# Kernel tuning notes

Measured on AMD Instinct MI355X. Metric: run time of the kernel, lower is better.

Reference implementation:

```python
import jax, jax.numpy as jnp
import numpy as np

B, C, H, W, D = 2, 256, 16, 16, 16
CQK = C // 8  # 32


def setup_inputs() -> dict:
    key = jax.random.key(0)
    ks = jax.random.split(key, 6)
    x = jax.random.normal(ks[0], (B, C, H, W, D), dtype=jnp.float32)
    wq = jax.random.normal(ks[1], (CQK, C), dtype=jnp.float32) * (1.0 / np.sqrt(C))
    wk = jax.random.normal(ks[2], (CQK, C), dtype=jnp.float32) * (1.0 / np.sqrt(C))
    wv = jax.random.normal(ks[3], (C, C), dtype=jnp.float32) * (1.0 / np.sqrt(C))
    bq = jnp.zeros((CQK,), dtype=jnp.float32)
    bk = jnp.zeros((CQK,), dtype=jnp.float32)
    bv = jnp.zeros((C,), dtype=jnp.float32)
    gamma_pam = jax.random.normal(ks[4], (1,), dtype=jnp.float32)
    gamma_cam = jax.random.normal(ks[5], (1,), dtype=jnp.float32)
    return {"x": x, "wq": wq, "bq": bq, "wk": wk, "bk": bk,
            "wv": wv, "bv": bv, "gamma_pam": gamma_pam, "gamma_cam": gamma_cam}


def _da_block(x, wq, bq, wk, bk, wv, bv, gamma_pam, gamma_cam):
    b, c, h, w, d = x.shape
    n = h * w * d
    xf = x.reshape(b, c, n)  # (B, C, N)

    # ---- PAM (position attention) ----
    # 1x1x1 Conv3d == per-voxel channel matmul
    q = jnp.einsum('oc,bcn->bon', wq, xf) + bq[None, :, None]  # (B, CQK, N)
    k = jnp.einsum('oc,bcn->bon', wk, xf) + bk[None, :, None]  # (B, CQK, N)
    v = jnp.einsum('oc,bcn->bon', wv, xf) + bv[None, :, None]  # (B, C, N)
    energy = jnp.einsum('bci,bcj->bij', q, k)                  # (B, N, N)
    attn = jax.nn.softmax(energy, axis=-1)
    # out[b,c,i] = sum_j v[b,c,j] * attn[b,i,j]
    pam_out = jnp.einsum('bcj,bij->bci', v, attn)              # (B, C, N)
    x1 = gamma_pam[0] * pam_out.reshape(b, c, h, w, d) + x

    # ---- CAM (channel attention, max-inverted energy) ----
    energy_c = jnp.einsum('bin,bjn->bij', xf, xf)              # (B, C, C)
    energy_new = jnp.max(energy_c, axis=-1, keepdims=True) - energy_c
    attn_c = jax.nn.softmax(energy_new, axis=-1)
    cam_out = jnp.einsum('bij,bjn->bin', attn_c, xf)           # (B, C, N)
    x2 = gamma_cam[0] * cam_out.reshape(b, c, h, w, d) + x

    return x1 + x2


def reference(x, wq, bq, wk, bk, wv, bv, gamma_pam, gamma_cam):
    return _da_block(x, wq, bq, wk, bk, wv, bv, gamma_pam, gamma_cam)
```

## Files before the change

### kernel.cpp

```cpp
#include <hip/hip_runtime.h>
#include <hip/hip_bf16.h>


#define B_ 2
#define C_ 256
#define N_ 4096
#define QK_ 32

#define TJ_ 128
#define PPB_ 136

typedef __hip_bfloat16 bf16;
typedef __attribute__((ext_vector_type(8))) short bf16x8f;
typedef __attribute__((ext_vector_type(4))) float f32x4;

union bf8pack { bf16 h[8]; int4 v; bf16x8f f; };
union bf4pack { bf16 h[4]; uint2 u; };

__global__ __launch_bounds__(256) void k_wcv(
    const float* __restrict__ wq, const float* __restrict__ wk, const float* __restrict__ wv,
    bf16* __restrict__ wqkh, bf16* __restrict__ wqkl,
    bf16* __restrict__ wvh, bf16* __restrict__ wvl) {
  int idx = blockIdx.x * 256 + threadIdx.x;
  if (idx < 64 * C_) {
    int r = idx >> 8, c = idx & 255;
    float v = (r < 32) ? wq[r * C_ + c] : wk[(r - 32) * C_ + c];
    bf16 h = __float2bfloat16(v);
    wqkh[idx] = h; wqkl[idx] = __float2bfloat16(v - __bfloat162float(h));
  } else {
    int j = idx - 64 * C_;
    float v = wv[j];
    bf16 h = __float2bfloat16(v);
    wvh[j] = h; wvl[j] = __float2bfloat16(v - __bfloat162float(h));
  }
}

__global__ __launch_bounds__(256) void k_xt(
    const float* __restrict__ x, bf16* __restrict__ xthi, bf16* __restrict__ xtlo,
    bf16* __restrict__ xchi, bf16* __restrict__ xclo) {
  int b = blockIdx.z;
  int c0 = blockIdx.y * 64;
  int n0 = blockIdx.x * 64;
  __shared__ float t[64 * 65];
  int tid = threadIdx.x;
  int col = tid & 63, rowq = tid >> 6;
#pragma unroll
  for (int k = 0; k < 16; k++) {
    int r = k * 4 + rowq;
    size_t src = ((size_t)b * C_ + c0 + r) * N_ + n0 + col;
    float v = x[src];
    t[r * 65 + col] = v;
    bf16 h = __float2bfloat16(v);
    xchi[src] = h;
    xclo[src] = __float2bfloat16(v - __bfloat162float(h));
  }
  __syncthreads();
#pragma unroll
  for (int k = 0; k < 16; k++) {
    int nrow = k * 4 + rowq;
    float v = t[col * 65 + nrow];
    bf16 h = __float2bfloat16(v);
    size_t o = ((size_t)b * N_ + n0 + nrow) * C_ + c0 + col;
    xthi[o] = h;
    xtlo[o] = __float2bfloat16(v - __bfloat162float(h));
  }
}

__global__ __launch_bounds__(256) void k_qkp(
    const bf16* __restrict__ xthi, const bf16* __restrict__ xtlo,
    const bf16* __restrict__ wqkh, const bf16* __restrict__ wqkl,
    const float* __restrict__ bq, const float* __restrict__ bk,
    bf16* __restrict__ qhi, bf16* __restrict__ qlo,
    bf16* __restrict__ khi, bf16* __restrict__ klo) {
  int b = blockIdx.y;
  int tid = threadIdx.x;
  int lane = tid & 63, wave = tid >> 6;
  int n16 = lane & 15, quad = lane >> 4;
  int nb = blockIdx.x * 32;

  f32x4 acc[2];
#pragma unroll
  for (int nt = 0; nt < 2; nt++) acc[nt] = (f32x4)(0.f);

#pragma unroll
  for (int kk = 0; kk < 8; kk++) {
    bf16x8f Ah, Al, Bh[2], Bl[2];
    {
      size_t off = (size_t)(wave * 16 + n16) * C_ + kk * 32 + quad * 8;
      Ah = *(const bf16x8f*)(const void*)(wqkh + off);
      Al = *(const bf16x8f*)(const void*)(wqkl + off);
    }
#pragma unroll
    for (int nt = 0; nt < 2; nt++) {
      size_t off = ((size_t)b * N_ + nb + nt * 16 + n16) * C_ + kk * 32 + quad * 8;
      Bh[nt] = *(const bf16x8f*)(const void*)(xthi + off);
      Bl[nt] = *(const bf16x8f*)(const void*)(xtlo + off);
    }
#pragma unroll
    for (int nt = 0; nt < 2; nt++) {
      acc[nt] = __builtin_amdgcn_mfma_f32_16x16x32_bf16(Ah, Bh[nt], acc[nt], 0, 0, 0);
      acc[nt] = __builtin_amdgcn_mfma_f32_16x16x32_bf16(Al, Bh[nt], acc[nt], 0, 0, 0);
      acc[nt] = __builtin_amdgcn_mfma_f32_16x16x32_bf16(Ah, Bl[nt], acc[nt], 0, 0, 0);
    }
  }
#pragma unroll
  for (int nt = 0; nt < 2; nt++) {
    int n = nb + nt * 16 + n16;
    int o0 = (wave & 1) * 16 + quad * 4;
    bf4pack ph, pl;
#pragma unroll
    for (int r = 0; r < 4; r++) {
      float v = acc[nt][r] + (wave < 2 ? bq[o0 + r] : bk[o0 + r]);
      bf16 h = __float2bfloat16(v);
      ph.h[r] = h; pl.h[r] = __float2bfloat16(v - __bfloat162float(h));
    }
    size_t base = ((size_t)b * N_ + n) * QK_ + o0;
    if (wave < 2) { *(uint2*)(qhi + base) = ph.u; *(uint2*)(qlo + base) = pl.u; }
    else          { *(uint2*)(khi + base) = ph.u; *(uint2*)(klo + base) = pl.u; }
  }
}

__global__ __launch_bounds__(256) void k_vbf2(
    const bf16* __restrict__ xthi, const bf16* __restrict__ xtlo,
    const bf16* __restrict__ wvh, const bf16* __restrict__ wvl,
    const float* __restrict__ bv, bf16* __restrict__ vbf) {
  int b = blockIdx.y;
  int n0 = blockIdx.x * 32;
  int tid = threadIdx.x;
  int lane = tid & 63, wave = tid >> 6;
  int n16 = lane & 15, quad = lane >> 4;
  int c0 = wave * 64;

  f32x4 acc[4][2];
#pragma unroll
  for (int ct = 0; ct < 4; ct++)
#pragma unroll
    for (int nt = 0; nt < 2; nt++) acc[ct][nt] = (f32x4)(0.f);

#pragma unroll
  for (int kk = 0; kk < 8; kk++) {
    bf16x8f Ah[4], Al[4], Bh[2], Bl[2];
#pragma unroll
    for (int ct = 0; ct < 4; ct++) {
      size_t off = (size_t)(c0 + ct * 16 + n16) * C_ + kk * 32 + quad * 8;
      Ah[ct] = *(const bf16x8f*)(const void*)(wvh + off);
      Al[ct] = *(const bf16x8f*)(const void*)(wvl + off);
    }
#pragma unroll
    for (int nt = 0; nt < 2; nt++) {
      size_t off = ((size_t)b * N_ + n0 + nt * 16 + n16) * C_ + kk * 32 + quad * 8;
      Bh[nt] = *(const bf16x8f*)(const void*)(xthi + off);
      Bl[nt] = *(const bf16x8f*)(const void*)(xtlo + off);
    }
#pragma unroll
    for (int ct = 0; ct < 4; ct++)
#pragma unroll
      for (int nt = 0; nt < 2; nt++) {
        acc[ct][nt] = __builtin_amdgcn_mfma_f32_16x16x32_bf16(Ah[ct], Bh[nt], acc[ct][nt], 0, 0, 0);
        acc[ct][nt] = __builtin_amdgcn_mfma_f32_16x16x32_bf16(Al[ct], Bh[nt], acc[ct][nt], 0, 0, 0);
        acc[ct][nt] = __builtin_amdgcn_mfma_f32_16x16x32_bf16(Ah[ct], Bl[nt], acc[ct][nt], 0, 0, 0);
      }
  }
#pragma unroll
  for (int ct = 0; ct < 4; ct++)
#pragma unroll
    for (int nt = 0; nt < 2; nt++) {
      int n = n0 + nt * 16 + n16;
      int cb = c0 + ct * 16 + quad * 4;
#pragma unroll
      for (int r = 0; r < 4; r++) {
        float v = acc[ct][nt][r] + bv[cb + r];
        vbf[((size_t)b * C_ + cb + r) * N_ + n] = __float2bfloat16(v);
      }
    }
}

__global__ __launch_bounds__(512) void k_pbm(
    const bf16* __restrict__ qhi, const bf16* __restrict__ qlo,
    const bf16* __restrict__ khi, const bf16* __restrict__ klo,
    const bf16* __restrict__ vbf,
    float* __restrict__ pamT) {
  int b = blockIdx.z;
  int h0 = blockIdx.y * 128;
  int i0 = blockIdx.x * 64;
  int tid = threadIdx.x;
  int lane = tid & 63, wave = tid >> 6;
  int n16 = lane & 15, quad = lane >> 4;

  __shared__ __align__(16) bf16 p_s[2][64 * PPB_];

  bf16x8f ahf[4], alf[4];
#pragma unroll
  for (int ih = 0; ih < 4; ih++) {
    size_t qoff = ((size_t)b * N_ + i0 + ih * 16 + n16) * QK_ + quad * 8;
    ahf[ih] = *(const bf16x8f*)(const void*)(qhi + qoff);
    alf[ih] = *(const bf16x8f*)(const void*)(qlo + qoff);
  }

  f32x4 acc[4];
  float l16[16];
#pragma unroll
  for (int ih = 0; ih < 4; ih++) acc[ih] = (f32x4)(0.f);
#pragma unroll
  for (int k = 0; k < 16; k++) l16[k] = 0.f;

  const bf16* khb = khi + ((size_t)b * N_ + wave * 16 + n16) * QK_ + quad * 8;
  const bf16* klb = klo + ((size_t)b * N_ + wave * 16 + n16) * QK_ + quad * 8;
  const bf16* vb0 = vbf + ((size_t)b * C_ + h0 + wave * 16 + n16) * N_ + quad * 8;

  const int NJT = N_ / TJ_;

  bf16x8f khf = *(const bf16x8f*)(const void*)khb;
  bf16x8f klf = *(const bf16x8f*)(const void*)klb;
  {
    bf16* pbuf = p_s[0];
#pragma unroll
    for (int ih = 0; ih < 4; ih++) {
      f32x4 t = (f32x4)(0.f);
      t = __builtin_amdgcn_mfma_f32_16x16x32_bf16(ahf[ih], khf, t, 0, 0, 0);
      t = __builtin_amdgcn_mfma_f32_16x16x32_bf16(alf[ih], khf, t, 0, 0, 0);
      t = __builtin_amdgcn_mfma_f32_16x16x32_bf16(ahf[ih], klf, t, 0, 0, 0);
#pragma unroll
      for (int r = 0; r < 4; r++) {
        int i = ih * 16 + quad * 4 + r;
        float p = __expf(t[r]);
        l16[ih * 4 + r] += p;
        pbuf[i * PPB_ + wave * 16 + n16] = __float2bfloat16(p);
      }
    }
  }
  khf = *(const bf16x8f*)(const void*)(khb + (size_t)TJ_ * QK_);
  klf = *(const bf16x8f*)(const void*)(klb + (size_t)TJ_ * QK_);
  bf16x8f vcur[4];
#pragma unroll
  for (int jhh = 0; jhh < 4; jhh++)
    vcur[jhh] = *(const bf16x8f*)(const void*)(vb0 + jhh * 32);
  __syncthreads();

  for (int jt = 0; jt < NJT; jt++) {
    f32x4 z[4];
    if (jt + 1 < NJT) {
#pragma unroll
      for (int ih = 0; ih < 4; ih++) {
        f32x4 t = (f32x4)(0.f);
        t = __builtin_amdgcn_mfma_f32_16x16x32_bf16(ahf[ih], khf, t, 0, 0, 0);
        t = __builtin_amdgcn_mfma_f32_16x16x32_bf16(alf[ih], khf, t, 0, 0, 0);
        t = __builtin_amdgcn_mfma_f32_16x16x32_bf16(ahf[ih], klf, t, 0, 0, 0);
        z[ih] = t;
      }
    }
    {
      const bf16* pbuf = p_s[jt & 1];
#pragma unroll
      for (int jhh = 0; jhh < 4; jhh++) {
        bf16x8f pa[4];
#pragma unroll
        for (int ih = 0; ih < 4; ih++)
          pa[ih] = *(const bf16x8f*)(const void*)(pbuf + (ih * 16 + n16) * PPB_ + jhh * 32 + quad * 8);
#pragma unroll
        for (int ih = 0; ih < 4; ih++)
          acc[ih] = __builtin_amdgcn_mfma_f32_16x16x32_bf16(pa[ih], vcur[jhh], acc[ih], 0, 0, 0);
      }
    }
    if (jt + 1 < NJT) {
      bf16* pbuf = p_s[(jt + 1) & 1];
#pragma unroll
      for (int ih = 0; ih < 4; ih++)
#pragma unroll
        for (int r = 0; r < 4; r++) {
          int i = ih * 16 + quad * 4 + r;
          float p = __expf(z[ih][r]);
          l16[ih * 4 + r] += p;
          pbuf[i * PPB_ + wave * 16 + n16] = __float2bfloat16(p);
        }
    }
    bf16x8f khn, kln, vnxt[4];
    if (jt + 2 < NJT) {
      size_t koff = (size_t)(jt + 2) * TJ_ * QK_;
      khn = *(const bf16x8f*)(const void*)(khb + koff);
      kln = *(const bf16x8f*)(const void*)(klb + koff);
    }
    if (jt + 1 < NJT) {
      int jb = (jt + 1) * TJ_;
#pragma unroll
      for (int jhh = 0; jhh < 4; jhh++)
        vnxt[jhh] = *(const bf16x8f*)(const void*)(vb0 + jb + jhh * 32);
    }
    __syncthreads();
    khf = khn; klf = kln;
#pragma unroll
    for (int jhh = 0; jhh < 4; jhh++) vcur[jhh] = vnxt[jhh];
  }

#pragma unroll
  for (int d = 1; d < 16; d <<= 1)
#pragma unroll
    for (int k = 0; k < 16; k++)
      l16[k] += __shfl_xor(l16[k], d, 64);
  float* red = (float*)p_s;
  float* linv = red + 8 * 64;
  if (n16 == 0) {
#pragma unroll
    for (int ih = 0; ih < 4; ih++)
#pragma unroll
      for (int r = 0; r < 4; r++)
        red[wave * 64 + ih * 16 + quad * 4 + r] = l16[ih * 4 + r];
  }
  __syncthreads();
  if (tid < 64) {
    float L = 0.f;
#pragma unroll
    for (int w = 0; w < 8; w++) L += red[w * 64 + tid];
    linv[tid] = 1.0f / L;
  }
  __syncthreads();
  int c = h0 + wave * 16 + n16;
#pragma unroll
  for (int ih = 0; ih < 4; ih++)
#pragma unroll
    for (int r = 0; r < 4; r++) {
      int i = ih * 16 + quad * 4 + r;
      pamT[((size_t)b * N_ + i0 + i) * C_ + c] = acc[ih][r] * linv[i];
    }
}

__global__ __launch_bounds__(256) void k_ce2(
    const bf16* __restrict__ xchi, const bf16* __restrict__ xclo,
    float* __restrict__ eCp) {
  int b = blockIdx.z;
  int kc = blockIdx.y;
  int it = blockIdx.x & 7, jh = blockIdx.x >> 3;
  int i0 = it * 32;
  int tid = threadIdx.x;
  int lane = tid & 63, wave = tid >> 6;
  int n16 = lane & 15, quad = lane >> 4;
  int j0 = jh * 128 + wave * 32;

  f32x4 acc[2][2];
#pragma unroll
  for (int it2 = 0; it2 < 2; it2++)
#pragma unroll
    for (int jt = 0; jt < 2; jt++) acc[it2][jt] = (f32x4)(0.f);

  size_t kb = (size_t)kc * 512;
#pragma unroll 2
  for (int kk = 0; kk < 16; kk++) {
    bf16x8f Ah[2], Al[2], Bh[2], Bl[2];
#pragma unroll
    for (int it2 = 0; it2 < 2; it2++) {
      size_t off = ((size_t)b * C_ + i0 + it2 * 16 + n16) * N_ + kb + kk * 32 + quad * 8;
      Ah[it2] = *(const bf16x8f*)(const void*)(xchi + off);
      Al[it2] = *(const bf16x8f*)(const void*)(xclo + off);
    }
#pragma unroll
    for (int jt = 0; jt < 2; jt++) {
      size_t off = ((size_t)b * C_ + j0 + jt * 16 + n16) * N_ + kb + kk * 32 + quad * 8;
      Bh[jt] = *(const bf16x8f*)(const void*)(xchi + off);
      Bl[jt] = *(const bf16x8f*)(const void*)(xclo + off);
    }
#pragma unroll
    for (int it2 = 0; it2 < 2; it2++)
#pragma unroll
      for (int jt = 0; jt < 2; jt++) {
        acc[it2][jt] = __builtin_amdgcn_mfma_f32_16x16x32_bf16(Ah[it2], Bh[jt], acc[it2][jt], 0, 0, 0);
        acc[it2][jt] = __builtin_amdgcn_mfma_f32_16x16x32_bf16(Al[it2], Bh[jt], acc[it2][jt], 0, 0, 0);
        acc[it2][jt] = __builtin_amdgcn_mfma_f32_16x16x32_bf16(Ah[it2], Bl[jt], acc[it2][jt], 0, 0, 0);
      }
  }
  float* dst = eCp + ((size_t)kc * B_ + b) * C_ * C_;
#pragma unroll
  for (int it2 = 0; it2 < 2; it2++)
#pragma unroll
    for (int jt = 0; jt < 2; jt++) {
      int i = i0 + it2 * 16 + quad * 4;
      int j = j0 + jt * 16 + n16;
#pragma unroll
      for (int r = 0; r < 4; r++)
        dst[(size_t)(i + r) * C_ + j] = acc[it2][jt][r];
    }
}

__global__ __launch_bounds__(256) void k_cs(
    const float* __restrict__ eCp, bf16* __restrict__ ahi) {
  int row = blockIdx.x;
  int b = row >> 8, i = row & 255;
  int j = threadIdx.x;
  float e = 0.f;
#pragma unroll
  for (int kc = 0; kc < 8; kc++) e += eCp[(((size_t)kc * B_ + b) * C_ + i) * C_ + j];
  float ne = -e;
  __shared__ float buf[256];
  buf[j] = ne;
  __syncthreads();
  for (int st = 128; st >= 1; st >>= 1) {
    if (j < st) buf[j] = fmaxf(buf[j], buf[j + st]);
    __syncthreads();
  }
  float m = buf[0];
  __syncthreads();
  float p = __expf(ne - m);
  buf[j] = p;
  __syncthreads();
  for (int st = 128; st >= 1; st >>= 1) {
    if (j < st) buf[j] += buf[j + st];
    __syncthreads();
  }
  ahi[(size_t)row * C_ + j] = __float2bfloat16(p / buf[0]);
}

__global__ __launch_bounds__(512) void k_cam(
    const bf16* __restrict__ xthi,
    const bf16* __restrict__ ahi,
    const float* __restrict__ pamT, const float* __restrict__ x,
    const float* __restrict__ gpam, const float* __restrict__ gcam,
    float* __restrict__ out) {
  int b = blockIdx.y;
  int n0 = blockIdx.x * 32;
  int tid = threadIdx.x;
  int lane = tid & 63, wave = tid >> 6;
  int n16 = lane & 15, quad = lane >> 4;
  int c0 = wave * 32;

  f32x4 acc[2][2];
#pragma unroll
  for (int nt = 0; nt < 2; nt++)
#pragma unroll
    for (int ct = 0; ct < 2; ct++) acc[nt][ct] = (f32x4)(0.f);

#pragma unroll
  for (int kk = 0; kk < 8; kk++) {
    bf16x8f Ah[2], Bh[2];
#pragma unroll
    for (int nt = 0; nt < 2; nt++) {
      size_t off = ((size_t)b * N_ + n0 + nt * 16 + n16) * C_ + kk * 32 + quad * 8;
      Ah[nt] = *(const bf16x8f*)(const void*)(xthi + off);
    }
#pragma unroll
    for (int ct = 0; ct < 2; ct++) {
      size_t off = ((size_t)b * C_ + c0 + ct * 16 + n16) * C_ + kk * 32 + quad * 8;
      Bh[ct] = *(const bf16x8f*)(const void*)(ahi + off);
    }
#pragma unroll
    for (int nt = 0; nt < 2; nt++)
#pragma unroll
      for (int ct = 0; ct < 2; ct++)
        acc[nt][ct] = __builtin_amdgcn_mfma_f32_16x16x32_bf16(Ah[nt], Bh[ct], acc[nt][ct], 0, 0, 0);
  }
  float gp = gpam[0], gc = gcam[0];
#pragma unroll
  for (int nt = 0; nt < 2; nt++)
#pragma unroll
    for (int ct = 0; ct < 2; ct++) {
      int c = c0 + ct * 16 + n16;
      int nb = n0 + nt * 16 + quad * 4;
      const float* xp = x + ((size_t)b * C_ + c) * N_ + nb;
      float4 x4 = *(const float4*)(const void*)xp;
      float4 o4;
      o4.x = gp * pamT[((size_t)b * N_ + nb + 0) * C_ + c] + gc * acc[nt][ct][0] + 2.0f * x4.x;
      o4.y = gp * pamT[((size_t)b * N_ + nb + 1) * C_ + c] + gc * acc[nt][ct][1] + 2.0f * x4.y;
      o4.z = gp * pamT[((size_t)b * N_ + nb + 2) * C_ + c] + gc * acc[nt][ct][2] + 2.0f * x4.z;
      o4.w = gp * pamT[((size_t)b * N_ + nb + 3) * C_ + c] + gc * acc[nt][ct][3] + 2.0f * x4.w;
      *(float4*)(out + ((size_t)b * C_ + c) * N_ + nb) = o4;
    }
}

extern "C" void kernel_launch(void* const* d_in, const int* in_sizes, int n_in,
                              void* d_out, int out_size, void* d_ws, size_t ws_size,
                              hipStream_t stream) {
  const float* x  = (const float*)d_in[0];
  const float* wq = (const float*)d_in[1];
  const float* bq = (const float*)d_in[2];
  const float* wk = (const float*)d_in[3];
  const float* bk = (const float*)d_in[4];
  const float* wv = (const float*)d_in[5];
  const float* bv = (const float*)d_in[6];
  const float* gp = (const float*)d_in[7];
  const float* gc = (const float*)d_in[8];
  float* out = (float*)d_out;

  float* ws = (float*)d_ws;
  size_t o = 0;
  float* pamT  = ws + o; o += (size_t)B_ * N_ * C_;
  float* mp    = ws + o; o += (size_t)2 * B_ * N_;
  float* lp    = ws + o; o += (size_t)2 * B_ * N_;
  float* eCp   = ws + o; o += (size_t)8 * B_ * C_ * C_;
  bf16*  ahi   = (bf16*)(ws + o); o += (size_t)B_ * C_ * C_ / 2;
  bf16*  alo   = (bf16*)(ws + o); o += (size_t)B_ * C_ * C_ / 2;
  bf16*  vbf   = (bf16*)(ws + o); o += (size_t)B_ * N_ * C_ / 2;
  bf16*  qhi   = (bf16*)(ws + o); o += (size_t)B_ * N_ * QK_ / 2;
  bf16*  qlo   = (bf16*)(ws + o); o += (size_t)B_ * N_ * QK_ / 2;
  bf16*  khi   = (bf16*)(ws + o); o += (size_t)B_ * N_ * QK_ / 2;
  bf16*  klo   = (bf16*)(ws + o); o += (size_t)B_ * N_ * QK_ / 2;
  float* xtbuf = ws + o; o += (size_t)2 * B_ * N_ * QK_ * 4;
  bf16* xthi = (bf16*)xtbuf;
  bf16* xtlo = (bf16*)(xtbuf + (size_t)B_ * N_ * C_ / 2);
  bf16* wqkh = (bf16*)eCp;
  bf16* wqkl = wqkh + (size_t)64 * C_;
  bf16* wvh  = wqkl + (size_t)64 * C_;
  bf16* wvl  = wvh + (size_t)C_ * C_;
  bf16* xchi = (bf16*)pamT;
  bf16* xclo = xchi + (size_t)B_ * C_ * N_;
  (void)mp; (void)lp; (void)alo;

  k_wcv<<<dim3((64 * C_ + C_ * C_) / 256), dim3(256), 0, stream>>>(wq, wk, wv, wqkh, wqkl, wvh, wvl);
  k_xt<<<dim3(N_ / 64, C_ / 64, B_), dim3(256), 0, stream>>>(x, xthi, xtlo, xchi, xclo);
  k_qkp<<<dim3(N_ / 32, B_), dim3(256), 0, stream>>>(xthi, xtlo, wqkh, wqkl, bq, bk, qhi, qlo, khi, klo);
  k_vbf2<<<dim3(N_ / 32, B_), dim3(256), 0, stream>>>(xthi, xtlo, wvh, wvl, bv, vbf);
  k_ce2<<<dim3(16, 8, B_), dim3(256), 0, stream>>>(xchi, xclo, eCp);
  k_cs<<<dim3(B_ * C_), dim3(256), 0, stream>>>(eCp, ahi);
  k_pbm<<<dim3(N_ / 64, 2, B_), dim3(512), 0, stream>>>(qhi, qlo, khi, klo, vbf, pamT);
  k_cam<<<dim3(N_ / 32, B_), dim3(512), 0, stream>>>(xthi, ahi, pamT, x, gp, gc, out);
}
```

Measured before the change: 179.6 us.

## Process two key tiles per barrier phase with XOR-swizzled P buffers

The PAM attention loop now handles two 128-column key tiles per phase, using four shared P buffers. This halves the number of __syncthreads per block. The padded P layout (stride 136) is replaced by an unpadded 128-stride layout with an XOR-style block rotation to avoid LDS bank conflicts. The cost is higher register pressure from double K and V prefetch registers and more LDS use, which may reduce occupancy.

Result: slower. 185.8 us (+3.5%).

```diff
diff --git a/kernel.cpp b/kernel.cpp
--- a/kernel.cpp
+++ b/kernel.cpp
@@ -187,7 +187,7 @@
   int lane = tid & 63, wave = tid >> 6;
   int n16 = lane & 15, quad = lane >> 4;
 
-  __shared__ __align__(16) bf16 p_s[2][64 * PPB_];
+  __shared__ __align__(16) bf16 p_s[4][64 * 128];
 
   bf16x8f ahf[4], alf[4];
 #pragma unroll
@@ -208,88 +208,120 @@
   const bf16* klb = klo + ((size_t)b * N_ + wave * 16 + n16) * QK_ + quad * 8;
   const bf16* vb0 = vbf + ((size_t)b * C_ + h0 + wave * 16 + n16) * N_ + quad * 8;
 
-  const int NJT = N_ / TJ_;
-
-  bf16x8f khf = *(const bf16x8f*)(const void*)khb;
-  bf16x8f klf = *(const bf16x8f*)(const void*)klb;
-  {
-    bf16* pbuf = p_s[0];
+  const int NPH = 16;
+  int wcol = wave * 16 + n16;
+  int wblk = wcol >> 3, wrem = wcol & 7;
+
+  bf16x8f khf[2], klf[2];
+#pragma unroll
+  for (int tt = 0; tt < 2; tt++) {
+    khf[tt] = *(const bf16x8f*)(const void*)(khb + (size_t)tt * TJ_ * QK_);
+    klf[tt] = *(const bf16x8f*)(const void*)(klb + (size_t)tt * TJ_ * QK_);
+  }
+#pragma unroll
+  for (int tt = 0; tt < 2; tt++) {
+    bf16* pbuf = p_s[tt];
 #pragma unroll
     for (int ih = 0; ih < 4; ih++) {
       f32x4 t = (f32x4)(0.f);
-      t = __builtin_amdgcn_mfma_f32_16x16x32_bf16(ahf[ih], khf, t, 0, 0, 0);
-      t = __builtin_amdgcn_mfma_f32_16x16x32_bf16(alf[ih], khf, t, 0, 0, 0);
-      t = __builtin_amdgcn_mfma_f32_16x16x32_bf16(ahf[ih], klf, t, 0, 0, 0);
+      t = __builtin_amdgcn_mfma_f32_16x16x32_bf16(ahf[ih], khf[tt], t, 0, 0, 0);
+      t = __builtin_amdgcn_mfma_f32_16x16x32_bf16(alf[ih], khf[tt], t, 0, 0, 0);
+      t = __builtin_amdgcn_mfma_f32_16x16x32_bf16(ahf[ih], klf[tt], t, 0, 0, 0);
 #pragma unroll
       for (int r = 0; r < 4; r++) {
         int i = ih * 16 + quad * 4 + r;
         float p = __expf(t[r]);
         l16[ih * 4 + r] += p;
-        pbuf[i * PPB_ + wave * 16 + n16] = __float2bfloat16(p);
-      }
-    }
-  }
-  khf = *(const bf16x8f*)(const void*)(khb + (size_t)TJ_ * QK_);
-  klf = *(const bf16x8f*)(const void*)(klb + (size_t)TJ_ * QK_);
-  bf16x8f vcur[4];
-#pragma unroll
-  for (int jhh = 0; jhh < 4; jhh++)
-    vcur[jhh] = *(const bf16x8f*)(const void*)(vb0 + jhh * 32);
-  __syncthreads();
-
-  for (int jt = 0; jt < NJT; jt++) {
-    f32x4 z[4];
-    if (jt + 1 < NJT) {
-#pragma unroll
-      for (int ih = 0; ih < 4; ih++) {
-        f32x4 t = (f32x4)(0.f);
-        t = __builtin_amdgcn_mfma_f32_16x16x32_bf16(ahf[ih], khf, t, 0, 0, 0);
-        t = __builtin_amdgcn_mfma_f32_16x16x32_bf16(alf[ih], khf, t, 0, 0, 0);
-        t = __builtin_amdgcn_mfma_f32_16x16x32_bf16(ahf[ih], klf, t, 0, 0, 0);
-        z[ih] = t;
-      }
-    }
-    {
-      const bf16* pbuf = p_s[jt & 1];
+        pbuf[i * 128 + (((wblk + i) & 15) << 3) + wrem] = __float2bfloat16(p);
+      }
+    }
+  }
+#pragma unroll
+  for (int tt = 0; tt < 2; tt++) {
+    khf[tt] = *(const bf16x8f*)(const void*)(khb + (size_t)(2 + tt) * TJ_ * QK_);
+    klf[tt] = *(const bf16x8f*)(const void*)(klb + (size_t)(2 + tt) * TJ_ * QK_);
+  }
+  bf16x8f vcur[2][4];
+#pragma unroll
+  for (int tt = 0; tt < 2; tt++)
+#pragma unroll
+    for (int jhh = 0; jhh < 4; jhh++)
+      vcur[tt][jhh] = *(const bf16x8f*)(const void*)(vb0 + (size_t)tt * TJ_ + jhh * 32);
+  __syncthreads();
+
+  for (int t = 0; t < NPH; t++) {
+    int pp = t & 1;
+    bf16* consume0 = p_s[pp * 2];
+    bf16* consume1 = p_s[pp * 2 + 1];
+    bf16* produce0 = p_s[(pp ^ 1) * 2];
+    bf16* produce1 = p_s[(pp ^ 1) * 2 + 1];
+    bool have_next = (t + 1 < NPH);
+
+#pragma unroll
+    for (int tt = 0; tt < 2; tt++) {
+      const bf16* cbuf = (tt == 0) ? consume0 : consume1;
+      bf16* pbuf = (tt == 0) ? produce0 : produce1;
+      f32x4 z[4];
+      if (have_next) {
+#pragma unroll
+        for (int ih = 0; ih < 4; ih++) {
+          f32x4 zz = (f32x4)(0.f);
+          zz = __builtin_amdgcn_mfma_f32_16x16x32_bf16(ahf[ih], khf[tt], zz, 0, 0, 0);
+          zz = __builtin_amdgcn_mfma_f32_16x16x32_bf16(alf[ih], khf[tt], zz, 0, 0, 0);
+          zz = __builtin_amdgcn_mfma_f32_16x16x32_bf16(ahf[ih], klf[tt], zz, 0, 0, 0);
+          z[ih] = zz;
+        }
+      }
 #pragma unroll
       for (int jhh = 0; jhh < 4; jhh++) {
+        int jb = jhh * 4 + quad;
         bf16x8f pa[4];
 #pragma unroll
+        for (int ih = 0; ih < 4; ih++) {
+          int ir = ih * 16 + n16;
+          pa[ih] = *(const bf16x8f*)(const void*)(cbuf + ir * 128 + (((jb + ir) & 15) << 3));
+        }
+#pragma unroll
         for (int ih = 0; ih < 4; ih++)
-          pa[ih] = *(const bf16x8f*)(const void*)(pbuf + (ih * 16 + n16) * PPB_ + jhh * 32 + quad * 8);
+          acc[ih] = __builtin_amdgcn_mfma_f32_16x16x32_bf16(pa[ih], vcur[tt][jhh], acc[ih], 0, 0, 0);
+      }
+      if (have_next) {
 #pragma unroll
         for (int ih = 0; ih < 4; ih++)
-          acc[ih] = __builtin_amdgcn_mfma_f32_16x16x32_bf16(pa[ih], vcur[jhh], acc[ih], 0, 0, 0);
-      }
-    }
-    if (jt + 1 < NJT) {
-      bf16* pbuf = p_s[(jt + 1) & 1];
-#pragma unroll
-      for (int ih = 0; ih < 4; ih++)
-#pragma unroll
-        for (int r = 0; r < 4; r++) {
-          int i = ih * 16 + quad * 4 + r;
-          float p = __expf(z[ih][r]);
-          l16[ih * 4 + r] += p;
-          pbuf[i * PPB_ + wave * 16 + n16] = __float2bfloat16(p);
-        }
-    }
-    bf16x8f khn, kln, vnxt[4];
-    if (jt + 2 < NJT) {
-      size_t koff = (size_t)(jt + 2) * TJ_ * QK_;
-      khn = *(const bf16x8f*)(const void*)(khb + koff);
-      kln = *(const bf16x8f*)(const void*)(klb + koff);
-    }
-    if (jt + 1 < NJT) {
-      int jb = (jt + 1) * TJ_;
-#pragma unroll
-      for (int jhh = 0; jhh < 4; jhh++)
-        vnxt[jhh] = *(const bf16x8f*)(const void*)(vb0 + jb + jhh * 32);
+#pragma unroll
+          for (int r = 0; r < 4; r++) {
+            int i = ih * 16 + quad * 4 + r;
+            float p = __expf(z[ih][r]);
+            l16[ih * 4 + r] += p;
+            pbuf[i * 128 + (((wblk + i) & 15) << 3) + wrem] = __float2bfloat16(p);
+          }
+      }
+    }
+    bf16x8f khn[2], kln[2], vnxt[2][4];
+    if (t + 2 < NPH) {
+#pragma unroll
+      for (int tt = 0; tt < 2; tt++) {
+        size_t koff = (size_t)(2 * (t + 2) + tt) * TJ_ * QK_;
+        khn[tt] = *(const bf16x8f*)(const void*)(khb + koff);
+        kln[tt] = *(const bf16x8f*)(const void*)(klb + koff);
+      }
+    }
+    if (have_next) {
+#pragma unroll
+      for (int tt = 0; tt < 2; tt++) {
+        size_t vb = (size_t)(2 * (t + 1) + tt) * TJ_;
+#pragma unroll
+        for (int jhh = 0; jhh < 4; jhh++)
+          vnxt[tt][jhh] = *(const bf16x8f*)(const void*)(vb0 + vb + jhh * 32);
+      }
     }
     __syncthreads();
-    khf = khn; klf = kln;
-#pragma unroll
-    for (int jhh = 0; jhh < 4; jhh++) vcur[jhh] = vnxt[jhh];
+#pragma unroll
+    for (int tt = 0; tt < 2; tt++) {
+      khf[tt] = khn[tt]; klf[tt] = kln[tt];
+#pragma unroll
+      for (int jhh = 0; jhh < 4; jhh++) vcur[tt][jhh] = vnxt[tt][jhh];
+    }
   }
 
 #pragma unroll
```
